# Performance work log

Measured on AMD Instinct MI355X. Metric: run time of the kernel, lower is better.

## Reference

```python
import jax, jax.numpy as jnp
import numpy as np
import math

B, N, C = 8, 512, 384
H, R = 6, 32
PAIR_HIDDEN = 16
RBF_K = 8
HEAD_SCALE = 1.0 / math.sqrt(R)


def setup_inputs() -> dict:
    key = jax.random.key(0)
    ks = jax.random.split(key, 16)
    s = 0.02
    inp = {
        'feats': jax.random.normal(ks[0], (B, 2 * N + 1, C), jnp.float32),
        'xy': jax.random.uniform(ks[1], (B, N, 2), jnp.float32),
        'Wq': jax.random.normal(ks[2], (C, H * R), jnp.float32) * s,
        'Wk': jax.random.normal(ks[3], (C, H * R), jnp.float32) * s,
        'Wpi': jax.random.normal(ks[4], (C, PAIR_HIDDEN), jnp.float32) * s,
        'bpi': jnp.zeros((PAIR_HIDDEN,), jnp.float32),
        'Wpj': jax.random.normal(ks[5], (C, PAIR_HIDDEN), jnp.float32) * s,
        'bpj': jnp.zeros((PAIR_HIDDEN,), jnp.float32),
        'alpha_pair': jnp.float32(0.5),
        'Wg1': jax.random.normal(ks[6], (2 + RBF_K + 2, 32), jnp.float32) * 0.3,
        'bg1': jnp.zeros((32,), jnp.float32),
        'Wg2': jax.random.normal(ks[7], (32, 1), jnp.float32) * 0.3,
        'bg2': jnp.zeros((1,), jnp.float32),
        'alpha_geom': jnp.float32(0.6),
        'Wa1': jax.random.normal(ks[8], (6, 16), jnp.float32) * 0.3,
        'ba1': jnp.zeros((16,), jnp.float32),
        'Wa2': jax.random.normal(ks[9], (16, 1), jnp.float32) * 0.3,
        'ba2': jnp.zeros((1,), jnp.float32),
        'alpha_angle': jnp.float32(0.6),
        'Wd': jax.random.normal(ks[10], (C, 1), jnp.float32) * s,
        'bd': jnp.zeros((1,), jnp.float32),
        'logit_scale': jnp.float32(1.0),
    }
    return inp


def _fold_vertices(feats):
    f = feats[:, 1:]                       # [B, 2N, C]
    b, l, c = f.shape
    return f.reshape(b, l // 2, 2, c).mean(axis=2)  # [B, N, C]


def _principal_orientation(xy):
    # PCA via 5-step power iteration; deterministic init (torch uses randn).
    b, n, _ = xy.shape
    X = xy - xy.mean(axis=1, keepdims=True)
    Cm = jnp.einsum('bnd,bne->bde', X, X) / (n + 1e-8)   # [B,2,2]
    v = jax.random.normal(jax.random.key(42), (b, 2, 1), xy.dtype)
    v = v / (jnp.linalg.norm(v, axis=1, keepdims=True) + 1e-8)
    for _ in range(5):
        v = Cm @ v
        v = v / (jnp.linalg.norm(v, axis=1, keepdims=True) + 1e-8)
    theta0 = jnp.arctan2(v[:, 1, 0], v[:, 0, 0])
    return theta0.reshape(b, 1, 1)


def reference(feats, xy, Wq, Wk, Wpi, bpi, Wpj, bpj, alpha_pair,
              Wg1, bg1, Wg2, bg2, alpha_geom, Wa1, ba1, Wa2, ba2, alpha_angle,
              Wd, bd, logit_scale):
    x = _fold_vertices(feats)                  # [B,N,C]
    b, n, c = x.shape

    Q = (x @ Wq).reshape(b, n, H, R)
    K = (x @ Wk).reshape(b, n, H, R)
    S = jnp.einsum('bnhr,bmhr->bnm', Q, K) * HEAD_SCALE   # heads summed

    a_i = jax.nn.relu(x @ Wpi + bpi)
    b_j = jax.nn.relu(x @ Wpj + bpj)
    S = S + jnp.maximum(alpha_pair, 0.0) * jnp.einsum('bnd,bmd->bnm', a_i, b_j)

    yv, xv = xy[..., 0], xy[..., 1]
    dy = yv[:, :, None] - yv[:, None, :]       # [B,N,N]
    dx = xv[:, :, None] - xv[:, None, :]
    theta = jnp.arctan2(dy, dx)
    theta0 = _principal_orientation(xy)
    theta = jnp.arctan2(jnp.sin(theta - theta0), jnp.cos(theta - theta0))

    # geometry bias
    rbf_mu = jnp.linspace(0.0, math.sqrt(2.0), RBF_K).astype(x.dtype)
    spacing = rbf_mu[1] - rbf_mu[0]
    rbf_gamma = 1.0 / (2.0 * spacing ** 2 + 1e-8)
    r = jnp.sqrt(dy * dy + dx * dx + 1e-8)
    phi = jnp.exp(-rbf_gamma * (r[..., None] - rbf_mu) ** 2)   # [B,N,N,K]
    c1, s1 = jnp.cos(theta), jnp.sin(theta)
    geom_feat = jnp.concatenate(
        [dy[..., None], dx[..., None], phi, c1[..., None], s1[..., None]], axis=-1)
    G = (jax.nn.relu(geom_feat @ Wg1 + bg1) @ Wg2 + bg2)[..., 0]
    S = S + jnp.maximum(alpha_geom, 0.0) * G

    # angle harmonics bias
    c2, s2 = jnp.cos(2.0 * theta), jnp.sin(2.0 * theta)
    c4, s4 = jnp.cos(4.0 * theta), jnp.sin(4.0 * theta)
    ang_feat = jnp.stack([c1, s1, c2, s2, c4, s4], axis=-1)    # [B,N,N,6]
    Hb = (jax.nn.relu(ang_feat @ Wa1 + ba1) @ Wa2 + ba2)[..., 0]
    S = S + jnp.maximum(alpha_angle, 0.0) * Hb

    d = (x @ Wd + bd)[..., 0]                  # [B,N]
    S = S + d[:, :, None] * jnp.eye(n, dtype=S.dtype)
    return S * jnp.maximum(logit_scale, 0.01)
```

## Files before the change

kernel.cpp:

```cpp
#include <hip/hip_runtime.h>
#include <hip/hip_bf16.h>
#include <stdint.h>
#include <string.h>
#include <math.h>

#define B_ 8
#define N_ 512
#define C_ 384
#define HR_ 192
#define PH_ 16
#define HEAD_SCALE_ 0.17677669529663687f

#define OFF_X   0
#define OFF_Q   (B_*N_*C_)
#define OFF_K   (OFF_Q + B_*N_*HR_)
#define OFF_A   (OFF_K + B_*N_*HR_)
#define OFF_BJ  (OFF_A + B_*N_*PH_)
#define OFF_D   (OFF_BJ + B_*N_*PH_)
#define OFF_CS  (OFF_D + B_*N_)
#define OFF_W   (OFF_CS + 2*B_)
#define OFF_FLAG (OFF_W + 700)
#define WS_FLOATS (OFF_W + 768)

struct VInit { float v[16]; };

__device__ __forceinline__ float cvt(ushort u) {
  union { uint32_t i; float f; } x; x.i = ((uint32_t)u) << 16; return x.f;
}
__device__ __forceinline__ float cvt(float f) { return f; }

__device__ __forceinline__ float4 ld4v(const ushort* p) {
  ushort4 u = *(const ushort4*)p;
  return make_float4(cvt(u.x), cvt(u.y), cvt(u.z), cvt(u.w));
}
__device__ __forceinline__ float4 ld4v(const float* p) { return *(const float4*)p; }

__global__ void detect_kernel(const uint32_t* __restrict__ wg1, float* __restrict__ ws) {
  if (threadIdx.x == 0 && blockIdx.x == 0) {
    int cnt = 0;
    for (int i = 0; i < 128; ++i) {
      uint32_t d = wg1[i];
      float v = cvt((ushort)(d & 0xFFFFu));
      float av = fabsf(v);
      if (av == 0.0f || (av >= 9.5367431640625e-07f && av <= 32.0f)) ++cnt;
    }
    *(int*)(ws + OFF_FLAG) = (cnt >= 64) ? 1 : 0;
  }
}

template <typename T>
__device__ void build_tables(const T* Wg1, const T* bg1, const T* Wg2, const T* bg2,
                             const T* Wa1, const T* ba1, const T* Wa2, const T* ba2,
                             const T* apair, const T* ageom, const T* aang, const T* lsc,
                             float* ws, int tid) {
  for (int j = tid; j < 32; j += 256) {
    float* wj = ws + OFF_W + j*16;
    #pragma unroll
    for (int i = 0; i < 12; ++i) wj[i] = cvt(Wg1[i*32 + j]);
    wj[12] = cvt(bg1[j]);
    wj[13] = cvt(Wg2[j]);
    wj[14] = 0.f; wj[15] = 0.f;
  }
  for (int j = tid; j < 16; j += 256) {
    float* wj = ws + OFF_W + 512 + j*8;
    #pragma unroll
    for (int i = 0; i < 6; ++i) wj[i] = cvt(Wa1[i*16 + j]);
    wj[6] = cvt(ba1[j]);
    wj[7] = cvt(Wa2[j]);
  }
  if (tid == 0) {
    ws[OFF_W + 640] = cvt(bg2[0]);
    ws[OFF_W + 641] = cvt(ba2[0]);
    ws[OFF_W + 642] = fmaxf(cvt(apair[0]), 0.f);
    ws[OFF_W + 643] = fmaxf(cvt(ageom[0]), 0.f);
    ws[OFF_W + 644] = fmaxf(cvt(aang[0]), 0.f);
    ws[OFF_W + 645] = fmaxf(cvt(lsc[0]), 0.01f);
  }
}

__global__ __launch_bounds__(256) void prep_kernel(
    const void* __restrict__ xy,
    const void* __restrict__ Wg1, const void* __restrict__ bg1,
    const void* __restrict__ Wg2, const void* __restrict__ bg2,
    const void* __restrict__ Wa1, const void* __restrict__ ba1,
    const void* __restrict__ Wa2, const void* __restrict__ ba2,
    const void* __restrict__ apair, const void* __restrict__ ageom,
    const void* __restrict__ aang, const void* __restrict__ lsc,
    float* __restrict__ ws, VInit vi)
{
  const int b = blockIdx.x, tid = threadIdx.x;
  const int bf = *(volatile const int*)(ws + OFF_FLAG);
  __shared__ float sxy[N_*2];
  __shared__ float red[256][4];

  if (bf) {
    const ushort* p = (const ushort*)xy + b*N_*2;
    for (int i = tid; i < N_*2; i += 256) sxy[i] = cvt(p[i]);
  } else {
    const float* p = (const float*)xy + b*N_*2;
    for (int i = tid; i < N_*2; i += 256) sxy[i] = p[i];
  }
  __syncthreads();

  float sy = 0.f, sx = 0.f;
  for (int i = tid; i < N_; i += 256) { sy += sxy[2*i]; sx += sxy[2*i+1]; }
  red[tid][0] = sy; red[tid][1] = sx;
  __syncthreads();
  for (int s = 128; s > 0; s >>= 1) {
    if (tid < s) { red[tid][0] += red[tid+s][0]; red[tid][1] += red[tid+s][1]; }
    __syncthreads();
  }
  const float my = red[0][0] / 512.0f;
  const float mx = red[0][1] / 512.0f;
  __syncthreads();

  float c00 = 0.f, c01 = 0.f, c11 = 0.f;
  for (int i = tid; i < N_; i += 256) {
    float y = sxy[2*i] - my;
    float x = sxy[2*i+1] - mx;
    c00 += y*y; c01 += y*x; c11 += x*x;
  }
  red[tid][0] = c00; red[tid][1] = c01; red[tid][2] = c11;
  __syncthreads();
  for (int s = 128; s > 0; s >>= 1) {
    if (tid < s) {
      red[tid][0] += red[tid+s][0];
      red[tid][1] += red[tid+s][1];
      red[tid][2] += red[tid+s][2];
    }
    __syncthreads();
  }
  if (tid == 0) {
    float C00 = red[0][0] / 512.0f, C01 = red[0][1] / 512.0f, C11 = red[0][2] / 512.0f;
    float v0 = vi.v[2*b], v1 = vi.v[2*b + 1];
    float nr = sqrtf(v0*v0 + v1*v1) + 1e-8f; v0 /= nr; v1 /= nr;
    for (int it = 0; it < 5; ++it) {
      float w0 = C00*v0 + C01*v1;
      float w1 = C01*v0 + C11*v1;
      nr = sqrtf(w0*w0 + w1*w1) + 1e-8f;
      v0 = w0/nr; v1 = w1/nr;
    }
    float h = sqrtf(v0*v0 + v1*v1);
    ws[OFF_CS + 2*b + 0] = v0 / h;
    ws[OFF_CS + 2*b + 1] = v1 / h;
  }

  if (b == 0) {
    if (bf) build_tables((const ushort*)Wg1, (const ushort*)bg1, (const ushort*)Wg2, (const ushort*)bg2,
                         (const ushort*)Wa1, (const ushort*)ba1, (const ushort*)Wa2, (const ushort*)ba2,
                         (const ushort*)apair, (const ushort*)ageom, (const ushort*)aang, (const ushort*)lsc,
                         ws, tid);
    else    build_tables((const float*)Wg1, (const float*)bg1, (const float*)Wg2, (const float*)bg2,
                         (const float*)Wa1, (const float*)ba1, (const float*)Wa2, (const float*)ba2,
                         (const float*)apair, (const float*)ageom, (const float*)aang, (const float*)lsc,
                         ws, tid);
  }
}

template <typename T>
__device__ __forceinline__ void fold_body(const T* feats, float* ws, int idx) {
  const int c4 = idx % 96;
  const int bn = idx / 96;
  const int n = bn & (N_ - 1), b = bn >> 9;
  const T* r1 = feats + ((size_t)(b*(2*N_+1) + 1 + 2*n))*C_ + c4*4;
  float4 a = ld4v(r1);
  float4 c = ld4v(r1 + C_);
  float4 o;
  o.x = 0.5f*(a.x + c.x); o.y = 0.5f*(a.y + c.y);
  o.z = 0.5f*(a.z + c.z); o.w = 0.5f*(a.w + c.w);
  *(float4*)(ws + OFF_X + (size_t)idx*4) = o;
}

__global__ __launch_bounds__(256) void fold_kernel(const void* __restrict__ feats,
                                                   float* __restrict__ ws) {
  const int idx = blockIdx.x * 256 + threadIdx.x;
  const int bf = *(volatile const int*)(ws + OFF_FLAG);
  if (bf) fold_body((const ushort*)feats, ws, idx);
  else    fold_body((const float*)feats, ws, idx);
}

#define PKC 32
#define PNKS (C_/PKC)
#define PLDW 68

template <typename T>
__device__ __forceinline__ float4 load_w_small(const T* Wpi, const T* Wpj,
                                               const T* Wd, int c, int wcq) {
  float v[4];
  #pragma unroll
  for (int k = 0; k < 4; ++k) {
    int col = wcq*4 + k;
    float f = 0.f;
    if (col < 16)      f = cvt(Wpi[c*PH_ + col]);
    else if (col < 32) f = cvt(Wpj[c*PH_ + (col - 16)]);
    else if (col == 32) f = cvt(Wd[c]);
    v[k] = f;
  }
  return make_float4(v[0], v[1], v[2], v[3]);
}

template <typename T>
__device__ void proj2_body(const T* __restrict__ Wq, const T* __restrict__ Wk,
                           const T* __restrict__ Wpi, const T* __restrict__ bpi,
                           const T* __restrict__ Wpj, const T* __restrict__ bpj,
                           const T* __restrict__ Wd,  const T* __restrict__ bd,
                           float* __restrict__ ws)
{
  const int ct  = blockIdx.x;
  const int rt  = blockIdx.y;
  const int tid = threadIdx.x;
  const int row0 = rt * 64;

  __shared__ float lx[PKC][PLDW];
  __shared__ float lw[PKC][PLDW];

  const float* X = ws + OFF_X + (size_t)row0 * C_;

  const bool sm = (ct == 6);
  const T* Wsrc = (ct < 3) ? Wq : Wk;
  const int col0 = (ct < 3) ? ct * 64 : (ct - 3) * 64;

  const int xrow = tid >> 3, xcq = tid & 7;
  const int wc   = tid >> 4, wcq = tid & 15;
  const int tr = tid >> 4, tc = tid & 15;

  float4 px0, px1, pw0, pw1;

  px0 = *(const float4*)(X + (size_t)(xrow     ) * C_ + xcq*4);
  px1 = *(const float4*)(X + (size_t)(xrow + 32) * C_ + xcq*4);
  if (!sm) {
    pw0 = ld4v(Wsrc + (size_t)(wc     ) * HR_ + col0 + wcq*4);
    pw1 = ld4v(Wsrc + (size_t)(wc + 16) * HR_ + col0 + wcq*4);
  } else {
    pw0 = load_w_small(Wpi, Wpj, Wd, wc,      wcq);
    pw1 = load_w_small(Wpi, Wpj, Wd, wc + 16, wcq);
  }

  float acc[4][4] = {{0,0,0,0},{0,0,0,0},{0,0,0,0},{0,0,0,0}};

  for (int ks = 0; ks < PNKS; ++ks) {
    lx[xcq*4+0][xrow]      = px0.x;
    lx[xcq*4+1][xrow]      = px0.y;
    lx[xcq*4+2][xrow]      = px0.z;
    lx[xcq*4+3][xrow]      = px0.w;
    lx[xcq*4+0][xrow + 32] = px1.x;
    lx[xcq*4+1][xrow + 32] = px1.y;
    lx[xcq*4+2][xrow + 32] = px1.z;
    lx[xcq*4+3][xrow + 32] = px1.w;
    *(float4*)&lw[wc     ][wcq*4] = pw0;
    *(float4*)&lw[wc + 16][wcq*4] = pw1;
    __syncthreads();

    if (ks + 1 < PNKS) {
      const int c0 = (ks + 1) * PKC;
      px0 = *(const float4*)(X + (size_t)(xrow     ) * C_ + c0 + xcq*4);
      px1 = *(const float4*)(X + (size_t)(xrow + 32) * C_ + c0 + xcq*4);
      if (!sm) {
        pw0 = ld4v(Wsrc + (size_t)(c0 + wc     ) * HR_ + col0 + wcq*4);
        pw1 = ld4v(Wsrc + (size_t)(c0 + wc + 16) * HR_ + col0 + wcq*4);
      } else {
        pw0 = load_w_small(Wpi, Wpj, Wd, c0 + wc,      wcq);
        pw1 = load_w_small(Wpi, Wpj, Wd, c0 + wc + 16, wcq);
      }
    }

    #pragma unroll
    for (int c = 0; c < PKC; ++c) {
      float4 xv = *(const float4*)&lx[c][tr*4];
      float4 wv = *(const float4*)&lw[c][tc*4];
      acc[0][0] = fmaf(xv.x, wv.x, acc[0][0]);
      acc[0][1] = fmaf(xv.x, wv.y, acc[0][1]);
      acc[0][2] = fmaf(xv.x, wv.z, acc[0][2]);
      acc[0][3] = fmaf(xv.x, wv.w, acc[0][3]);
      acc[1][0] = fmaf(xv.y, wv.x, acc[1][0]);
      acc[1][1] = fmaf(xv.y, wv.y, acc[1][1]);
      acc[1][2] = fmaf(xv.y, wv.z, acc[1][2]);
      acc[1][3] = fmaf(xv.y, wv.w, acc[1][3]);
      acc[2][0] = fmaf(xv.z, wv.x, acc[2][0]);
      acc[2][1] = fmaf(xv.z, wv.y, acc[2][1]);
      acc[2][2] = fmaf(xv.z, wv.z, acc[2][2]);
      acc[2][3] = fmaf(xv.z, wv.w, acc[2][3]);
      acc[3][0] = fmaf(xv.w, wv.x, acc[3][0]);
      acc[3][1] = fmaf(xv.w, wv.y, acc[3][1]);
      acc[3][2] = fmaf(xv.w, wv.z, acc[3][2]);
      acc[3][3] = fmaf(xv.w, wv.w, acc[3][3]);
    }
    __syncthreads();
  }

  if (!sm) {
    float* base = ws + ((ct < 3) ? OFF_Q : OFF_K);
    #pragma unroll
    for (int r = 0; r < 4; ++r) {
      const int row = row0 + tr*4 + r;
      *(float4*)(base + (size_t)row * HR_ + col0 + tc*4) =
          make_float4(acc[r][0], acc[r][1], acc[r][2], acc[r][3]);
    }
  } else {
    #pragma unroll
    for (int r = 0; r < 4; ++r) {
      const int row = row0 + tr*4 + r;
      #pragma unroll
      for (int k = 0; k < 4; ++k) {
        const int col = tc*4 + k;
        if (col < 16) {
          ws[OFF_A + (size_t)row * PH_ + col] =
              fmaxf(acc[r][k] + cvt(bpi[col]), 0.f);
        } else if (col < 32) {
          ws[OFF_BJ + (size_t)row * PH_ + (col - 16)] =
              fmaxf(acc[r][k] + cvt(bpj[col - 16]), 0.f);
        } else if (col == 32) {
          ws[OFF_D + row] = acc[r][k] + cvt(bd[0]);
        }
      }
    }
  }
}

__global__ __launch_bounds__(256) void proj_kernel(
    const void* __restrict__ Wq, const void* __restrict__ Wk,
    const void* __restrict__ Wpi, const void* __restrict__ bpi,
    const void* __restrict__ Wpj, const void* __restrict__ bpj,
    const void* __restrict__ Wd,  const void* __restrict__ bd,
    float* __restrict__ ws)
{
  const int bf = *(volatile const int*)(ws + OFF_FLAG);
  if (bf) proj2_body((const ushort*)Wq, (const ushort*)Wk, (const ushort*)Wpi, (const ushort*)bpi,
                     (const ushort*)Wpj, (const ushort*)bpj, (const ushort*)Wd, (const ushort*)bd, ws);
  else    proj2_body((const float*)Wq, (const float*)Wk, (const float*)Wpi, (const float*)bpi,
                     (const float*)Wpj, (const float*)bpj, (const float*)Wd, (const float*)bd, ws);
}

__global__ __launch_bounds__(256, 2) void score_kernel(
    const void* __restrict__ xy, const float* __restrict__ ws,
    void* __restrict__ out)
{
  const int b  = blockIdx.z;
  const int n0 = blockIdx.y * 32, m0 = blockIdx.x * 32;
  const int tid = threadIdx.x;
  const int bf = *(volatile const int*)(ws + OFF_FLAG);

  __shared__ float Qt[32][196];
  __shared__ float Kt[32][196];
  __shared__ float At[32][20];
  __shared__ float Bt[32][20];
  __shared__ float xyn[32][2], xym[32][2], dn[32];

  const float* Qg = ws + OFF_Q + ((size_t)(b*N_) + n0) * HR_;
  const float* Kg = ws + OFF_K + ((size_t)(b*N_) + m0) * HR_;
  for (int i = tid; i < 1536; i += 256) {
    int row = i / 48, c = (i % 48) * 4;
    *(float4*)&Qt[row][c] = *(const float4*)(Qg + row*HR_ + c);
    *(float4*)&Kt[row][c] = *(const float4*)(Kg + row*HR_ + c);
  }
  const float* Ag = ws + OFF_A  + ((size_t)(b*N_) + n0) * PH_;
  const float* Bg = ws + OFF_BJ + ((size_t)(b*N_) + m0) * PH_;
  for (int i = tid; i < 128; i += 256) {
    int row = i / 4, c = (i % 4) * 4;
    *(float4*)&At[row][c] = *(const float4*)(Ag + row*PH_ + c);
    *(float4*)&Bt[row][c] = *(const float4*)(Bg + row*PH_ + c);
  }
  if (bf) {
    const ushort* p = (const ushort*)xy;
    if (tid < 32) {
      xyn[tid][0] = cvt(p[((b*N_) + n0 + tid)*2 + 0]);
      xyn[tid][1] = cvt(p[((b*N_) + n0 + tid)*2 + 1]);
      xym[tid][0] = cvt(p[((b*N_) + m0 + tid)*2 + 0]);
      xym[tid][1] = cvt(p[((b*N_) + m0 + tid)*2 + 1]);
      dn[tid] = ws[OFF_D + b*N_ + n0 + tid];
    }
  } else {
    const float* p = (const float*)xy;
    if (tid < 32) {
      xyn[tid][0] = p[((b*N_) + n0 + tid)*2 + 0];
      xyn[tid][1] = p[((b*N_) + n0 + tid)*2 + 1];
      xym[tid][0] = p[((b*N_) + m0 + tid)*2 + 0];
      xym[tid][1] = p[((b*N_) + m0 + tid)*2 + 1];
      dn[tid] = ws[OFF_D + b*N_ + n0 + tid];
    }
  }
  __syncthreads();

  const float c0 = ws[OFF_CS + 2*b], s0 = ws[OFF_CS + 2*b + 1];
  const float* wsm = ws + OFF_W;
  const float bg2v = wsm[640], ba2v = wsm[641];
  const float ap = wsm[642], ag = wsm[643], aa = wsm[644], ls = wsm[645];

  const int nl = tid >> 3, mg = tid & 7;

  float accQ[4] = {0,0,0,0}, accP[4] = {0,0,0,0};
  #pragma unroll 4
  for (int c = 0; c < HR_; c += 4) {
    float4 q = *(const float4*)&Qt[nl][c];
    #pragma unroll
    for (int p = 0; p < 4; ++p) {
      float4 k = *(const float4*)&Kt[mg + 8*p][c];
      accQ[p] = fmaf(q.x,k.x, fmaf(q.y,k.y, fmaf(q.z,k.z, fmaf(q.w,k.w, accQ[p]))));
    }
  }
  #pragma unroll
  for (int c = 0; c < PH_; c += 4) {
    float4 a = *(const float4*)&At[nl][c];
    #pragma unroll
    for (int p = 0; p < 4; ++p) {
      float4 v = *(const float4*)&Bt[mg + 8*p][c];
      accP[p] = fmaf(a.x,v.x, fmaf(a.y,v.y, fmaf(a.z,v.z, fmaf(a.w,v.w, accP[p]))));
    }
  }

  const float STEP  = 1.41421354f / 7.0f;
  const float GAMMA = 1.0f / (2.0f*STEP*STEP + 1e-8f);
  const float yn = xyn[nl][0], xn = xyn[nl][1];
  float DY[4], DX[4], C1[4], S1[4], C2[4], S2[4], C4v[4], S4[4], PHI[4][8];
  #pragma unroll
  for (int p = 0; p < 4; ++p) {
    int ml = mg + 8*p;
    float dy = yn - xym[ml][0], dx = xn - xym[ml][1];
    DY[p] = dy; DX[p] = dx;
    float h2 = fmaf(dx, dx, dy*dy);
    float r = sqrtf(h2 + 1e-8f);
    float ct, st;
    if (h2 > 0.f) { float ih = 1.0f / sqrtf(h2); ct = dx*ih; st = dy*ih; }
    else          { ct = 1.f; st = 0.f; }
    float c1 = ct*c0 + st*s0;
    float s1 = st*c0 - ct*s0;
    C1[p] = c1; S1[p] = s1;
    float c2 = c1*c1 - s1*s1, s2 = 2.f*c1*s1;
    C2[p] = c2; S2[p] = s2;
    C4v[p] = c2*c2 - s2*s2; S4[p] = 2.f*c2*s2;
    #pragma unroll
    for (int k = 0; k < 8; ++k) {
      float d = r - (float)k * STEP;
      PHI[p][k] = __expf(-GAMMA * d * d);
    }
  }

  float g[4] = {0,0,0,0};
  #pragma unroll 4
  for (int j = 0; j < 32; ++j) {
    const float* wj = wsm + j*16;
    #pragma unroll
    for (int p = 0; p < 4; ++p) {
      float h = fmaf(DY[p], wj[0], fmaf(DX[p], wj[1], wj[12]));
      #pragma unroll
      for (int k = 0; k < 8; ++k) h = fmaf(PHI[p][k], wj[2+k], h);
      h = fmaf(C1[p], wj[10], fmaf(S1[p], wj[11], h));
      g[p] = fmaf(fmaxf(h, 0.f), wj[13], g[p]);
    }
  }

  float hb[4] = {0,0,0,0};
  #pragma unroll 4
  for (int j = 0; j < 16; ++j) {
    const float* wj = wsm + 512 + j*8;
    #pragma unroll
    for (int p = 0; p < 4; ++p) {
      float h = fmaf(C1[p],  wj[0], fmaf(S1[p], wj[1], wj[6]));
      h = fmaf(C2[p],  wj[2], fmaf(S2[p], wj[3], h));
      h = fmaf(C4v[p], wj[4], fmaf(S4[p], wj[5], h));
      hb[p] = fmaf(fmaxf(h, 0.f), wj[7], hb[p]);
    }
  }

  const int n_g = n0 + nl;
  #pragma unroll
  for (int p = 0; p < 4; ++p) {
    const int m_g = m0 + mg + 8*p;
    float S = HEAD_SCALE_*accQ[p] + ap*accP[p] + ag*(g[p] + bg2v) + aa*(hb[p] + ba2v);
    if (n_g == m_g) S += dn[nl];
    S *= ls;
    const size_t oi = ((size_t)(b*N_) + n_g)*N_ + m_g;
    if (bf) ((__hip_bfloat16*)out)[oi] = __float2bfloat16(S);
    else    ((float*)out)[oi] = S;
  }
}

static inline uint32_t rotl32(uint32_t x, int d) { return (x << d) | (x >> (32 - d)); }

static void threefry2x32_host(uint32_t k0, uint32_t k1, uint32_t& x0, uint32_t& x1) {
  const uint32_t ks0 = k0, ks1 = k1, ks2 = k0 ^ k1 ^ 0x1BD11BDAu;
  static const int R[2][4] = {{13,15,26,6},{17,29,16,24}};
  x0 += ks0; x1 += ks1;
  const uint32_t ks[3] = {ks0, ks1, ks2};
  for (int i = 0; i < 5; ++i) {
    const int* r = R[i & 1];
    for (int j = 0; j < 4; ++j) { x0 += x1; x1 = rotl32(x1, r[j]); x1 ^= x0; }
    x0 += ks[(i + 1) % 3];
    x1 += ks[(i + 2) % 3] + (uint32_t)(i + 1);
  }
}

static float erfinv_host(float x) {
  float w = -log1pf(-x * x);
  float p;
  if (w < 5.0f) {
    w = w - 2.5f;
    p = 2.81022636e-08f;
    p = fmaf(p, w, 3.43273939e-07f);
    p = fmaf(p, w, -3.5233877e-06f);
    p = fmaf(p, w, -4.39150654e-06f);
    p = fmaf(p, w, 0.00021858087f);
    p = fmaf(p, w, -0.00125372503f);
    p = fmaf(p, w, -0.00417768164f);
    p = fmaf(p, w, 0.246640727f);
    p = fmaf(p, w, 1.50140941f);
  } else {
    w = sqrtf(w) - 3.0f;
    p = -0.000200214257f;
    p = fmaf(p, w, 0.000100950558f);
    p = fmaf(p, w, 0.00134934322f);
    p = fmaf(p, w, -0.00367342844f);
    p = fmaf(p, w, 0.00573950773f);
    p = fmaf(p, w, -0.0076224613f);
    p = fmaf(p, w, 0.00943887047f);
    p = fmaf(p, w, 1.00167406f);
    p = fmaf(p, w, 2.83297682f);
  }
  return p * x;
}

static VInit make_vinit() {
  VInit vi;
  for (int i = 0; i < 16; ++i) {
    uint32_t o0 = 0u, o1 = (uint32_t)i;
    threefry2x32_host(0u, 42u, o0, o1);
    uint32_t bits = o0 ^ o1;
    uint32_t fb = (bits >> 9) | 0x3f800000u;
    float f; memcpy(&f, &fb, 4); f -= 1.0f;
    const float lo = -0.99999994f;
    float u = f * 2.0f + lo;
    if (u < lo) u = lo;
    vi.v[i] = 1.41421354f * erfinv_host(u);
  }
  return vi;
}

extern "C" void kernel_launch(void* const* d_in, const int* in_sizes, int n_in,
                              void* d_out, int out_size, void* d_ws, size_t ws_size,
                              hipStream_t stream) {
  (void)in_sizes; (void)n_in; (void)out_size;
  if (ws_size < (size_t)WS_FLOATS * sizeof(float)) return;

  const void* feats = d_in[0];
  const void* xy    = d_in[1];
  const void* Wq    = d_in[2];
  const void* Wk    = d_in[3];
  const void* Wpi   = d_in[4];
  const void* bpi   = d_in[5];
  const void* Wpj   = d_in[6];
  const void* bpj   = d_in[7];
  const void* apair = d_in[8];
  const void* Wg1   = d_in[9];
  const void* bg1   = d_in[10];
  const void* bg2w  = d_in[11];
  const void* bg2b  = d_in[12];
  const void* ageom = d_in[13];
  const void* Wa1   = d_in[14];
  const void* ba1   = d_in[15];
  const void* Wa2   = d_in[16];
  const void* ba2   = d_in[17];
  const void* aang  = d_in[18];
  const void* Wd    = d_in[19];
  const void* bd    = d_in[20];
  const void* lsc   = d_in[21];
  float* ws = (float*)d_ws;

  VInit vi = make_vinit();

  hipLaunchKernelGGL(detect_kernel, dim3(1), dim3(64), 0, stream,
      (const uint32_t*)Wg1, ws);
  hipLaunchKernelGGL(prep_kernel, dim3(B_), dim3(256), 0, stream,
      xy, Wg1, bg1, bg2w, bg2b, Wa1, ba1, Wa2, ba2, apair, ageom, aang, lsc, ws, vi);
  hipLaunchKernelGGL(fold_kernel, dim3(1536), dim3(256), 0, stream, feats, ws);
  hipLaunchKernelGGL(proj_kernel, dim3(7, 64), dim3(256), 0, stream,
      Wq, Wk, Wpi, bpi, Wpj, bpj, Wd, bd, ws);
  hipLaunchKernelGGL(score_kernel, dim3(16, 16, B_), dim3(256), 0, stream,
      xy, ws, d_out);
}
```

Measured before the change: 223.7 us.

## Use bf16 MFMA for QK and pair scores in score kernel when inputs are bf16

When the inputs are bf16, the projection stage now writes Q and K as bf16 with a 224-wide row: the head scale is folded into Q, and the pair features (pre-scaled by alpha_pair), along with zero padding, are appended as extra K-dimension columns. A new score kernel computes the combined QK plus pair term with seven 16x16x32 bf16 MFMA instructions per wave instead of staging fp32 tiles in LDS and doing scalar FMAs. It then evaluates the geometry and angle MLPs in the MFMA output layout. This removes LDS staging and scalar dot-product work, at the cost of rounding Q and K to bf16 and launching an extra kernel that exits early for the fp32 path.

```diff
diff --git a/kernel.cpp b/kernel.cpp
--- a/kernel.cpp
+++ b/kernel.cpp
@@ -10,6 +10,7 @@
 #define HR_ 192
 #define PH_ 16
 #define HEAD_SCALE_ 0.17677669529663687f
+#define QK2W_ 224
 
 #define OFF_X   0
 #define OFF_Q   (B_*N_*C_)
@@ -24,10 +25,18 @@
 
 struct VInit { float v[16]; };
 
+typedef __attribute__((ext_vector_type(8))) short short8v;
+typedef __attribute__((ext_vector_type(4))) float f32x4;
+
 __device__ __forceinline__ float cvt(ushort u) {
   union { uint32_t i; float f; } x; x.i = ((uint32_t)u) << 16; return x.f;
 }
 __device__ __forceinline__ float cvt(float f) { return f; }
+
+__device__ __forceinline__ ushort f2bf(float f) {
+  __hip_bfloat16 h = __float2bfloat16(f);
+  union { __hip_bfloat16 b; ushort u; } x; x.b = h; return x.u;
+}
 
 __device__ __forceinline__ float4 ld4v(const ushort* p) {
   ushort4 u = *(const ushort4*)p;
@@ -288,29 +297,70 @@
     __syncthreads();
   }
 
-  if (!sm) {
-    float* base = ws + ((ct < 3) ? OFF_Q : OFF_K);
-    #pragma unroll
-    for (int r = 0; r < 4; ++r) {
-      const int row = row0 + tr*4 + r;
-      *(float4*)(base + (size_t)row * HR_ + col0 + tc*4) =
-          make_float4(acc[r][0], acc[r][1], acc[r][2], acc[r][3]);
+  if constexpr (sizeof(T) == 2) {
+    ushort* q2 = (ushort*)(ws + OFF_Q);
+    ushort* k2 = (ushort*)(ws + OFF_K);
+    if (!sm) {
+      ushort* base = (ct < 3) ? q2 : k2;
+      const float sc = (ct < 3) ? HEAD_SCALE_ : 1.0f;
+      #pragma unroll
+      for (int r = 0; r < 4; ++r) {
+        const int row = row0 + tr*4 + r;
+        ushort4 o = make_ushort4(f2bf(sc*acc[r][0]), f2bf(sc*acc[r][1]),
+                                 f2bf(sc*acc[r][2]), f2bf(sc*acc[r][3]));
+        *(ushort4*)(base + (size_t)row*QK2W_ + col0 + tc*4) = o;
+      }
+    } else {
+      {
+        const int row = row0 + (tid >> 2), ch = tid & 3;
+        ushort4 z = make_ushort4(0,0,0,0);
+        *(ushort4*)(q2 + (size_t)row*QK2W_ + 208 + ch*4) = z;
+        *(ushort4*)(k2 + (size_t)row*QK2W_ + 208 + ch*4) = z;
+      }
+      const float ap = ws[OFF_W + 642];
+      #pragma unroll
+      for (int r = 0; r < 4; ++r) {
+        const int row = row0 + tr*4 + r;
+        #pragma unroll
+        for (int k = 0; k < 4; ++k) {
+          const int col = tc*4 + k;
+          if (col < 16) {
+            q2[(size_t)row*QK2W_ + 192 + col] =
+                f2bf(ap * fmaxf(acc[r][k] + cvt(bpi[col]), 0.f));
+          } else if (col < 32) {
+            k2[(size_t)row*QK2W_ + 192 + (col - 16)] =
+                f2bf(fmaxf(acc[r][k] + cvt(bpj[col - 16]), 0.f));
+          } else if (col == 32) {
+            ws[OFF_D + row] = acc[r][k] + cvt(bd[0]);
+          }
+        }
+      }
     }
   } else {
-    #pragma unroll
-    for (int r = 0; r < 4; ++r) {
-      const int row = row0 + tr*4 + r;
+    if (!sm) {
+      float* base = ws + ((ct < 3) ? OFF_Q : OFF_K);
       #pragma unroll
-      for (int k = 0; k < 4; ++k) {
-        const int col = tc*4 + k;
-        if (col < 16) {
-          ws[OFF_A + (size_t)row * PH_ + col] =
-              fmaxf(acc[r][k] + cvt(bpi[col]), 0.f);
-        } else if (col < 32) {
-          ws[OFF_BJ + (size_t)row * PH_ + (col - 16)] =
-              fmaxf(acc[r][k] + cvt(bpj[col - 16]), 0.f);
-        } else if (col == 32) {
-          ws[OFF_D + row] = acc[r][k] + cvt(bd[0]);
+      for (int r = 0; r < 4; ++r) {
+        const int row = row0 + tr*4 + r;
+        *(float4*)(base + (size_t)row * HR_ + col0 + tc*4) =
+            make_float4(acc[r][0], acc[r][1], acc[r][2], acc[r][3]);
+      }
+    } else {
+      #pragma unroll
+      for (int r = 0; r < 4; ++r) {
+        const int row = row0 + tr*4 + r;
+        #pragma unroll
+        for (int k = 0; k < 4; ++k) {
+          const int col = tc*4 + k;
+          if (col < 16) {
+            ws[OFF_A + (size_t)row * PH_ + col] =
+                fmaxf(acc[r][k] + cvt(bpi[col]), 0.f);
+          } else if (col < 32) {
+            ws[OFF_BJ + (size_t)row * PH_ + (col - 16)] =
+                fmaxf(acc[r][k] + cvt(bpj[col - 16]), 0.f);
+          } else if (col == 32) {
+            ws[OFF_D + row] = acc[r][k] + cvt(bd[0]);
+          }
         }
       }
     }
@@ -331,14 +381,124 @@
                      (const float*)Wpj, (const float*)bpj, (const float*)Wd, (const float*)bd, ws);
 }
 
-__global__ __launch_bounds__(256, 2) void score_kernel(
+__global__ __launch_bounds__(256) void score_bf16_kernel(
     const void* __restrict__ xy, const float* __restrict__ ws,
     void* __restrict__ out)
 {
+  if (*(volatile const int*)(ws + OFF_FLAG) == 0) return;
   const int b  = blockIdx.z;
   const int n0 = blockIdx.y * 32, m0 = blockIdx.x * 32;
   const int tid = threadIdx.x;
-  const int bf = *(volatile const int*)(ws + OFF_FLAG);
+
+  __shared__ float xyn[32][2], xym[32][2], dn[32];
+  if (tid < 32) {
+    const ushort* p = (const ushort*)xy;
+    xyn[tid][0] = cvt(p[((b*N_) + n0 + tid)*2 + 0]);
+    xyn[tid][1] = cvt(p[((b*N_) + n0 + tid)*2 + 1]);
+    xym[tid][0] = cvt(p[((b*N_) + m0 + tid)*2 + 0]);
+    xym[tid][1] = cvt(p[((b*N_) + m0 + tid)*2 + 1]);
+    dn[tid] = ws[OFF_D + b*N_ + n0 + tid];
+  }
+  __syncthreads();
+
+  const int w  = tid >> 6, l = tid & 63;
+  const int wr = w >> 1, wc = w & 1;
+  const int lr = l & 15, lk = l >> 4;
+
+  const ushort* Qg = (const ushort*)(ws + OFF_Q)
+      + ((size_t)(b*N_) + n0 + wr*16 + lr) * QK2W_ + lk*8;
+  const ushort* Kg = (const ushort*)(ws + OFF_K)
+      + ((size_t)(b*N_) + m0 + wc*16 + lr) * QK2W_ + lk*8;
+
+  f32x4 acc = {0.f, 0.f, 0.f, 0.f};
+  #pragma unroll
+  for (int kc = 0; kc < 7; ++kc) {
+    short8v av = *(const short8v*)(Qg + kc*32);
+    short8v bv = *(const short8v*)(Kg + kc*32);
+    acc = __builtin_amdgcn_mfma_f32_16x16x32_bf16(av, bv, acc, 0, 0, 0);
+  }
+
+  const float c0 = ws[OFF_CS + 2*b], s0 = ws[OFF_CS + 2*b + 1];
+  const float* wsm = ws + OFF_W;
+  const float bg2v = wsm[640], ba2v = wsm[641];
+  const float ag = wsm[643], aa = wsm[644], ls = wsm[645];
+
+  const int ml = wc*16 + lr;
+  const float ym = xym[ml][0], xm = xym[ml][1];
+
+  const float STEP  = 1.41421354f / 7.0f;
+  const float GAMMA = 1.0f / (2.0f*STEP*STEP + 1e-8f);
+  float C1[4], S1[4], C2[4], S2[4], C4v[4], S4[4], DY[4], DX[4], PHI[4][8];
+  #pragma unroll
+  for (int r = 0; r < 4; ++r) {
+    const int nl_ = wr*16 + lk*4 + r;
+    float dy = xyn[nl_][0] - ym, dx = xyn[nl_][1] - xm;
+    DY[r] = dy; DX[r] = dx;
+    float h2 = fmaf(dx, dx, dy*dy);
+    float rr = sqrtf(h2 + 1e-8f);
+    float ct, st;
+    if (h2 > 0.f) { float ih = 1.0f / sqrtf(h2); ct = dx*ih; st = dy*ih; }
+    else          { ct = 1.f; st = 0.f; }
+    float c1 = ct*c0 + st*s0;
+    float s1 = st*c0 - ct*s0;
+    C1[r] = c1; S1[r] = s1;
+    float c2 = c1*c1 - s1*s1, s2 = 2.f*c1*s1;
+    C2[r] = c2; S2[r] = s2;
+    C4v[r] = c2*c2 - s2*s2; S4[r] = 2.f*c2*s2;
+    #pragma unroll
+    for (int k = 0; k < 8; ++k) {
+      float d = rr - (float)k * STEP;
+      PHI[r][k] = __expf(-GAMMA * d * d);
+    }
+  }
+
+  float g[4] = {0,0,0,0};
+  #pragma unroll 4
+  for (int j = 0; j < 32; ++j) {
+    const float* wj = wsm + j*16;
+    #pragma unroll
+    for (int r = 0; r < 4; ++r) {
+      float h = fmaf(DY[r], wj[0], fmaf(DX[r], wj[1], wj[12]));
+      #pragma unroll
+      for (int k = 0; k < 8; ++k) h = fmaf(PHI[r][k], wj[2+k], h);
+      h = fmaf(C1[r], wj[10], fmaf(S1[r], wj[11], h));
+      g[r] = fmaf(fmaxf(h, 0.f), wj[13], g[r]);
+    }
+  }
+
+  float hb[4] = {0,0,0,0};
+  #pragma unroll 4
+  for (int j = 0; j < 16; ++j) {
+    const float* wj = wsm + 512 + j*8;
+    #pragma unroll
+    for (int r = 0; r < 4; ++r) {
+      float h = fmaf(C1[r],  wj[0], fmaf(S1[r], wj[1], wj[6]));
+      h = fmaf(C2[r],  wj[2], fmaf(S2[r], wj[3], h));
+      h = fmaf(C4v[r], wj[4], fmaf(S4[r], wj[5], h));
+      hb[r] = fmaf(fmaxf(h, 0.f), wj[7], hb[r]);
+    }
+  }
+
+  const int m_g = m0 + ml;
+  #pragma unroll
+  for (int r = 0; r < 4; ++r) {
+    const int nl_ = wr*16 + lk*4 + r;
+    const int n_g = n0 + nl_;
+    float S = acc[r] + ag*(g[r] + bg2v) + aa*(hb[r] + ba2v);
+    if (n_g == m_g) S += dn[nl_];
+    S *= ls;
+    ((__hip_bfloat16*)out)[((size_t)(b*N_) + n_g)*N_ + m_g] = __float2bfloat16(S);
+  }
+}
+
+__global__ __launch_bounds__(256, 2) void score_f32_kernel(
+    const void* __restrict__ xy, const float* __restrict__ ws,
+    void* __restrict__ out)
+{
+  if (*(volatile const int*)(ws + OFF_FLAG) != 0) return;
+  const int b  = blockIdx.z;
+  const int n0 = blockIdx.y * 32, m0 = blockIdx.x * 32;
+  const int tid = threadIdx.x;
 
   __shared__ float Qt[32][196];
   __shared__ float Kt[32][196];
@@ -360,16 +520,7 @@
     *(float4*)&At[row][c] = *(const float4*)(Ag + row*PH_ + c);
     *(float4*)&Bt[row][c] = *(const float4*)(Bg + row*PH_ + c);
   }
-  if (bf) {
-    const ushort* p = (const ushort*)xy;
-    if (tid < 32) {
-      xyn[tid][0] = cvt(p[((b*N_) + n0 + tid)*2 + 0]);
-      xyn[tid][1] = cvt(p[((b*N_) + n0 + tid)*2 + 1]);
-      xym[tid][0] = cvt(p[((b*N_) + m0 + tid)*2 + 0]);
-      xym[tid][1] = cvt(p[((b*N_) + m0 + tid)*2 + 1]);
-      dn[tid] = ws[OFF_D + b*N_ + n0 + tid];
-    }
-  } else {
+  {
     const float* p = (const float*)xy;
     if (tid < 32) {
       xyn[tid][0] = p[((b*N_) + n0 + tid)*2 + 0];
@@ -469,9 +620,7 @@
     float S = HEAD_SCALE_*accQ[p] + ap*accP[p] + ag*(g[p] + bg2v) + aa*(hb[p] + ba2v);
     if (n_g == m_g) S += dn[nl];
     S *= ls;
-    const size_t oi = ((size_t)(b*N_) + n_g)*N_ + m_g;
-    if (bf) ((__hip_bfloat16*)out)[oi] = __float2bfloat16(S);
-    else    ((float*)out)[oi] = S;
+    ((float*)out)[((size_t)(b*N_) + n_g)*N_ + m_g] = S;
   }
 }
 
@@ -574,6 +723,8 @@
   hipLaunchKernelGGL(fold_kernel, dim3(1536), dim3(256), 0, stream, feats, ws);
   hipLaunchKernelGGL(proj_kernel, dim3(7, 64), dim3(256), 0, stream,
       Wq, Wk, Wpi, bpi, Wpj, bpj, Wd, bd, ws);
-  hipLaunchKernelGGL(score_kernel, dim3(16, 16, B_), dim3(256), 0, stream,
+  hipLaunchKernelGGL(score_bf16_kernel, dim3(16, 16, B_), dim3(256), 0, stream,
       xy, ws, d_out);
-}
+  hipLaunchKernelGGL(score_f32_kernel, dim3(16, 16, B_), dim3(256), 0, stream,
+      xy, ws, d_out);
+}
```

After: 222.0 us. About the same (-0.8%).

## Compute QK and pair scores with split-bf16 MFMA instead of FP32 FMA

Applied to the files above, without the earlier changes.

The projection kernel now writes Q (pre-scaled by head scale) and K as hi/lo bf16 pairs in a 224-wide row. The pair features, with alpha_pair folded into the query side, are packed into columns 192-207 and zero-padded to 224. The score kernel drops the shared-memory FP32 dot products and computes each 16x16 tile with three bf16 MFMA calls per K chunk (hh, hl, lh), approximating FP32 accuracy. This removes the LDS staging and scalar FMA loops, in exchange for some precision loss from the dropped lo*lo term and a changed thread-to-output mapping for the geometry MLP.

```diff
diff --git a/kernel.cpp b/kernel.cpp
--- a/kernel.cpp
+++ b/kernel.cpp
@@ -10,24 +10,34 @@
 #define HR_ 192
 #define PH_ 16
 #define HEAD_SCALE_ 0.17677669529663687f
-
-#define OFF_X   0
-#define OFF_Q   (B_*N_*C_)
-#define OFF_K   (OFF_Q + B_*N_*HR_)
-#define OFF_A   (OFF_K + B_*N_*HR_)
-#define OFF_BJ  (OFF_A + B_*N_*PH_)
-#define OFF_D   (OFF_BJ + B_*N_*PH_)
-#define OFF_CS  (OFF_D + B_*N_)
-#define OFF_W   (OFF_CS + 2*B_)
+#define QK2W_ 224
+
+#define QK2SZF  (B_*N_*QK2W_/2)
+#define OFF_X    0
+#define OFF_Q2   (B_*N_*C_)
+#define OFF_Q2L  (OFF_Q2  + QK2SZF)
+#define OFF_K2   (OFF_Q2L + QK2SZF)
+#define OFF_K2L  (OFF_K2  + QK2SZF)
+#define OFF_D    (OFF_K2L + QK2SZF)
+#define OFF_CS   (OFF_D + B_*N_)
+#define OFF_W    (OFF_CS + 2*B_)
 #define OFF_FLAG (OFF_W + 700)
 #define WS_FLOATS (OFF_W + 768)
 
 struct VInit { float v[16]; };
 
+typedef __attribute__((ext_vector_type(8))) short short8v;
+typedef __attribute__((ext_vector_type(4))) float f32x4;
+
 __device__ __forceinline__ float cvt(ushort u) {
   union { uint32_t i; float f; } x; x.i = ((uint32_t)u) << 16; return x.f;
 }
 __device__ __forceinline__ float cvt(float f) { return f; }
+
+__device__ __forceinline__ ushort f2bf(float f) {
+  __hip_bfloat16 h = __float2bfloat16(f);
+  union { __hip_bfloat16 b; ushort u; } x; x.b = h; return x.u;
+}
 
 __device__ __forceinline__ float4 ld4v(const ushort* p) {
   ushort4 u = *(const ushort4*)p;
@@ -197,6 +207,11 @@
     v[k] = f;
   }
   return make_float4(v[0], v[1], v[2], v[3]);
+}
+
+__device__ __forceinline__ void split_bf(float v, ushort& hi, ushort& lo) {
+  hi = f2bf(v);
+  lo = f2bf(v - cvt(hi));
 }
 
 template <typename T>
@@ -288,15 +303,35 @@
     __syncthreads();
   }
 
+  ushort* q2h = (ushort*)(ws + OFF_Q2);
+  ushort* q2l = (ushort*)(ws + OFF_Q2L);
+  ushort* k2h = (ushort*)(ws + OFF_K2);
+  ushort* k2l = (ushort*)(ws + OFF_K2L);
+
   if (!sm) {
-    float* base = ws + ((ct < 3) ? OFF_Q : OFF_K);
+    const float sc = (ct < 3) ? HEAD_SCALE_ : 1.0f;
+    ushort* bh = (ct < 3) ? q2h : k2h;
+    ushort* bl = (ct < 3) ? q2l : k2l;
     #pragma unroll
     for (int r = 0; r < 4; ++r) {
       const int row = row0 + tr*4 + r;
-      *(float4*)(base + (size_t)row * HR_ + col0 + tc*4) =
-          make_float4(acc[r][0], acc[r][1], acc[r][2], acc[r][3]);
+      ushort4 oh, ol;
+      split_bf(sc*acc[r][0], oh.x, ol.x);
+      split_bf(sc*acc[r][1], oh.y, ol.y);
+      split_bf(sc*acc[r][2], oh.z, ol.z);
+      split_bf(sc*acc[r][3], oh.w, ol.w);
+      *(ushort4*)(bh + (size_t)row*QK2W_ + col0 + tc*4) = oh;
+      *(ushort4*)(bl + (size_t)row*QK2W_ + col0 + tc*4) = ol;
     }
   } else {
+    {
+      const int row = row0 + (tid & 63);
+      ushort* arr = (tid < 64) ? q2h : (tid < 128) ? q2l : (tid < 192) ? k2h : k2l;
+      uint4 z = make_uint4(0,0,0,0);
+      *(uint4*)(arr + (size_t)row*QK2W_ + 208) = z;
+      *(uint4*)(arr + (size_t)row*QK2W_ + 216) = z;
+    }
+    const float ap = ws[OFF_W + 642];
     #pragma unroll
     for (int r = 0; r < 4; ++r) {
       const int row = row0 + tr*4 + r;
@@ -304,11 +339,15 @@
       for (int k = 0; k < 4; ++k) {
         const int col = tc*4 + k;
         if (col < 16) {
-          ws[OFF_A + (size_t)row * PH_ + col] =
-              fmaxf(acc[r][k] + cvt(bpi[col]), 0.f);
+          float v = ap * fmaxf(acc[r][k] + cvt(bpi[col]), 0.f);
+          ushort hi, lo; split_bf(v, hi, lo);
+          q2h[(size_t)row*QK2W_ + 192 + col] = hi;
+          q2l[(size_t)row*QK2W_ + 192 + col] = lo;
         } else if (col < 32) {
-          ws[OFF_BJ + (size_t)row * PH_ + (col - 16)] =
-              fmaxf(acc[r][k] + cvt(bpj[col - 16]), 0.f);
+          float v = fmaxf(acc[r][k] + cvt(bpj[col - 16]), 0.f);
+          ushort hi, lo; split_bf(v, hi, lo);
+          k2h[(size_t)row*QK2W_ + 192 + (col - 16)] = hi;
+          k2l[(size_t)row*QK2W_ + 192 + (col - 16)] = lo;
         } else if (col == 32) {
           ws[OFF_D + row] = acc[r][k] + cvt(bd[0]);
         }
@@ -331,107 +370,88 @@
                      (const float*)Wpj, (const float*)bpj, (const float*)Wd, (const float*)bd, ws);
 }
 
-__global__ __launch_bounds__(256, 2) void score_kernel(
+__global__ __launch_bounds__(256) void score_kernel(
     const void* __restrict__ xy, const float* __restrict__ ws,
     void* __restrict__ out)
 {
+  const int bf = *(volatile const int*)(ws + OFF_FLAG);
   const int b  = blockIdx.z;
   const int n0 = blockIdx.y * 32, m0 = blockIdx.x * 32;
   const int tid = threadIdx.x;
-  const int bf = *(volatile const int*)(ws + OFF_FLAG);
-
-  __shared__ float Qt[32][196];
-  __shared__ float Kt[32][196];
-  __shared__ float At[32][20];
-  __shared__ float Bt[32][20];
+
   __shared__ float xyn[32][2], xym[32][2], dn[32];
-
-  const float* Qg = ws + OFF_Q + ((size_t)(b*N_) + n0) * HR_;
-  const float* Kg = ws + OFF_K + ((size_t)(b*N_) + m0) * HR_;
-  for (int i = tid; i < 1536; i += 256) {
-    int row = i / 48, c = (i % 48) * 4;
-    *(float4*)&Qt[row][c] = *(const float4*)(Qg + row*HR_ + c);
-    *(float4*)&Kt[row][c] = *(const float4*)(Kg + row*HR_ + c);
-  }
-  const float* Ag = ws + OFF_A  + ((size_t)(b*N_) + n0) * PH_;
-  const float* Bg = ws + OFF_BJ + ((size_t)(b*N_) + m0) * PH_;
-  for (int i = tid; i < 128; i += 256) {
-    int row = i / 4, c = (i % 4) * 4;
-    *(float4*)&At[row][c] = *(const float4*)(Ag + row*PH_ + c);
-    *(float4*)&Bt[row][c] = *(const float4*)(Bg + row*PH_ + c);
-  }
-  if (bf) {
-    const ushort* p = (const ushort*)xy;
-    if (tid < 32) {
+  if (tid < 32) {
+    if (bf) {
+      const ushort* p = (const ushort*)xy;
       xyn[tid][0] = cvt(p[((b*N_) + n0 + tid)*2 + 0]);
       xyn[tid][1] = cvt(p[((b*N_) + n0 + tid)*2 + 1]);
       xym[tid][0] = cvt(p[((b*N_) + m0 + tid)*2 + 0]);
       xym[tid][1] = cvt(p[((b*N_) + m0 + tid)*2 + 1]);
-      dn[tid] = ws[OFF_D + b*N_ + n0 + tid];
-    }
-  } else {
-    const float* p = (const float*)xy;
-    if (tid < 32) {
+    } else {
+      const float* p = (const float*)xy;
       xyn[tid][0] = p[((b*N_) + n0 + tid)*2 + 0];
       xyn[tid][1] = p[((b*N_) + n0 + tid)*2 + 1];
       xym[tid][0] = p[((b*N_) + m0 + tid)*2 + 0];
       xym[tid][1] = p[((b*N_) + m0 + tid)*2 + 1];
-      dn[tid] = ws[OFF_D + b*N_ + n0 + tid];
-    }
+    }
+    dn[tid] = ws[OFF_D + b*N_ + n0 + tid];
   }
   __syncthreads();
+
+  const int w  = tid >> 6, l = tid & 63;
+  const int wr = w >> 1, wc = w & 1;
+  const int lr = l & 15, lk = l >> 4;
+
+  const size_t qoff = ((size_t)(b*N_) + n0 + wr*16 + lr) * QK2W_ + lk*8;
+  const size_t koff = ((size_t)(b*N_) + m0 + wc*16 + lr) * QK2W_ + lk*8;
+  const ushort* qh = (const ushort*)(ws + OFF_Q2)  + qoff;
+  const ushort* ql = (const ushort*)(ws + OFF_Q2L) + qoff;
+  const ushort* kh = (const ushort*)(ws + OFF_K2)  + koff;
+  const ushort* kl = (const ushort*)(ws + OFF_K2L) + koff;
+
+  f32x4 acc = {0.f, 0.f, 0.f, 0.f};
+  #pragma unroll
+  for (int kc = 0; kc < 7; ++kc) {
+    short8v ah = *(const short8v*)(qh + kc*32);
+    short8v al = *(const short8v*)(ql + kc*32);
+    short8v bh = *(const short8v*)(kh + kc*32);
+    short8v bl = *(const short8v*)(kl + kc*32);
+    acc = __builtin_amdgcn_mfma_f32_16x16x32_bf16(ah, bh, acc, 0, 0, 0);
+    acc = __builtin_amdgcn_mfma_f32_16x16x32_bf16(ah, bl, acc, 0, 0, 0);
+    acc = __builtin_amdgcn_mfma_f32_16x16x32_bf16(al, bh, acc, 0, 0, 0);
+  }
 
   const float c0 = ws[OFF_CS + 2*b], s0 = ws[OFF_CS + 2*b + 1];
   const float* wsm = ws + OFF_W;
   const float bg2v = wsm[640], ba2v = wsm[641];
-  const float ap = wsm[642], ag = wsm[643], aa = wsm[644], ls = wsm[645];
-
-  const int nl = tid >> 3, mg = tid & 7;
-
-  float accQ[4] = {0,0,0,0}, accP[4] = {0,0,0,0};
-  #pragma unroll 4
-  for (int c = 0; c < HR_; c += 4) {
-    float4 q = *(const float4*)&Qt[nl][c];
-    #pragma unroll
-    for (int p = 0; p < 4; ++p) {
-      float4 k = *(const float4*)&Kt[mg + 8*p][c];
-      accQ[p] = fmaf(q.x,k.x, fmaf(q.y,k.y, fmaf(q.z,k.z, fmaf(q.w,k.w, accQ[p]))));
-    }
-  }
-  #pragma unroll
-  for (int c = 0; c < PH_; c += 4) {
-    float4 a = *(const float4*)&At[nl][c];
-    #pragma unroll
-    for (int p = 0; p < 4; ++p) {
-      float4 v = *(const float4*)&Bt[mg + 8*p][c];
-      accP[p] = fmaf(a.x,v.x, fmaf(a.y,v.y, fmaf(a.z,v.z, fmaf(a.w,v.w, accP[p]))));
-    }
-  }
+  const float ag = wsm[643], aa = wsm[644], ls = wsm[645];
+
+  const int ml = wc*16 + lr;
+  const float ym = xym[ml][0], xm = xym[ml][1];
 
   const float STEP  = 1.41421354f / 7.0f;
   const float GAMMA = 1.0f / (2.0f*STEP*STEP + 1e-8f);
-  const float yn = xyn[nl][0], xn = xyn[nl][1];
-  float DY[4], DX[4], C1[4], S1[4], C2[4], S2[4], C4v[4], S4[4], PHI[4][8];
+  float C1[4], S1[4], C2[4], S2[4], C4v[4], S4[4], DY[4], DX[4], PHI[4][8];
   #pragma unroll
-  for (int p = 0; p < 4; ++p) {
-    int ml = mg + 8*p;
-    float dy = yn - xym[ml][0], dx = xn - xym[ml][1];
-    DY[p] = dy; DX[p] = dx;
+  for (int r = 0; r < 4; ++r) {
+    const int nl_ = wr*16 + lk*4 + r;
+    float dy = xyn[nl_][0] - ym, dx = xyn[nl_][1] - xm;
+    DY[r] = dy; DX[r] = dx;
     float h2 = fmaf(dx, dx, dy*dy);
-    float r = sqrtf(h2 + 1e-8f);
+    float rr = sqrtf(h2 + 1e-8f);
     float ct, st;
     if (h2 > 0.f) { float ih = 1.0f / sqrtf(h2); ct = dx*ih; st = dy*ih; }
     else          { ct = 1.f; st = 0.f; }
     float c1 = ct*c0 + st*s0;
     float s1 = st*c0 - ct*s0;
-    C1[p] = c1; S1[p] = s1;
+    C1[r] = c1; S1[r] = s1;
     float c2 = c1*c1 - s1*s1, s2 = 2.f*c1*s1;
-    C2[p] = c2; S2[p] = s2;
-    C4v[p] = c2*c2 - s2*s2; S4[p] = 2.f*c2*s2;
+    C2[r] = c2; S2[r] = s2;
+    C4v[r] = c2*c2 - s2*s2; S4[r] = 2.f*c2*s2;
     #pragma unroll
     for (int k = 0; k < 8; ++k) {
-      float d = r - (float)k * STEP;
-      PHI[p][k] = __expf(-GAMMA * d * d);
+      float d = rr - (float)k * STEP;
+      PHI[r][k] = __expf(-GAMMA * d * d);
     }
   }
 
@@ -440,12 +460,12 @@
   for (int j = 0; j < 32; ++j) {
     const float* wj = wsm + j*16;
     #pragma unroll
-    for (int p = 0; p < 4; ++p) {
-      float h = fmaf(DY[p], wj[0], fmaf(DX[p], wj[1], wj[12]));
+    for (int r = 0; r < 4; ++r) {
+      float h = fmaf(DY[r], wj[0], fmaf(DX[r], wj[1], wj[12]));
       #pragma unroll
-      for (int k = 0; k < 8; ++k) h = fmaf(PHI[p][k], wj[2+k], h);
-      h = fmaf(C1[p], wj[10], fmaf(S1[p], wj[11], h));
-      g[p] = fmaf(fmaxf(h, 0.f), wj[13], g[p]);
+      for (int k = 0; k < 8; ++k) h = fmaf(PHI[r][k], wj[2+k], h);
+      h = fmaf(C1[r], wj[10], fmaf(S1[r], wj[11], h));
+      g[r] = fmaf(fmaxf(h, 0.f), wj[13], g[r]);
     }
   }
 
@@ -454,20 +474,21 @@
   for (int j = 0; j < 16; ++j) {
     const float* wj = wsm + 512 + j*8;
     #pragma unroll
-    for (int p = 0; p < 4; ++p) {
-      float h = fmaf(C1[p],  wj[0], fmaf(S1[p], wj[1], wj[6]));
-      h = fmaf(C2[p],  wj[2], fmaf(S2[p], wj[3], h));
-      h = fmaf(C4v[p], wj[4], fmaf(S4[p], wj[5], h));
-      hb[p] = fmaf(fmaxf(h, 0.f), wj[7], hb[p]);
-    }
-  }
-
-  const int n_g = n0 + nl;
+    for (int r = 0; r < 4; ++r) {
+      float h = fmaf(C1[r],  wj[0], fmaf(S1[r], wj[1], wj[6]));
+      h = fmaf(C2[r],  wj[2], fmaf(S2[r], wj[3], h));
+      h = fmaf(C4v[r], wj[4], fmaf(S4[r], wj[5], h));
+      hb[r] = fmaf(fmaxf(h, 0.f), wj[7], hb[r]);
+    }
+  }
+
+  const int m_g = m0 + ml;
   #pragma unroll
-  for (int p = 0; p < 4; ++p) {
-    const int m_g = m0 + mg + 8*p;
-    float S = HEAD_SCALE_*accQ[p] + ap*accP[p] + ag*(g[p] + bg2v) + aa*(hb[p] + ba2v);
-    if (n_g == m_g) S += dn[nl];
+  for (int r = 0; r < 4; ++r) {
+    const int nl_ = wr*16 + lk*4 + r;
+    const int n_g = n0 + nl_;
+    float S = acc[r] + ag*(g[r] + bg2v) + aa*(hb[r] + ba2v);
+    if (n_g == m_g) S += dn[nl_];
     S *= ls;
     const size_t oi = ((size_t)(b*N_) + n_g)*N_ + m_g;
     if (bf) ((__hip_bfloat16*)out)[oi] = __float2bfloat16(S);
```

Result: faster. 201.2 us (-10.1%).
